# Kernel optimization log

Hardware: AMD Instinct MI355X
Metric: run time of the kernel (lower is better)

Reference implementation:

```python
import jax, jax.numpy as jnp
import numpy as np

D = 512; N = 1536; H = 4; DH = D // H
MAX_INT = 5; BINS = 100; LAYERS = 3


def _mha(q_in, k_in, v_in, in_w, in_b, out_w, out_b):
    """PyTorch-style nn.MultiheadAttention (batch of 1). Returns (out [Nq,D], head-avg weights [Nq,Nk])."""
    wq, wk, wv = in_w[:D], in_w[D:2 * D], in_w[2 * D:]
    bq, bk, bv = in_b[:D], in_b[D:2 * D], in_b[2 * D:]
    n_q, n_k = q_in.shape[0], k_in.shape[0]
    q = (q_in @ wq.T + bq).reshape(n_q, H, DH).transpose(1, 0, 2)  # [H,Nq,dh]
    k = (k_in @ wk.T + bk).reshape(n_k, H, DH).transpose(1, 0, 2)
    v = (v_in @ wv.T + bv).reshape(n_k, H, DH).transpose(1, 0, 2)
    scores = jnp.einsum('hqd,hkd->hqk', q, k) / jnp.sqrt(jnp.asarray(DH, q.dtype))
    w = jax.nn.softmax(scores, axis=-1)  # [H,Nq,Nk]
    out = jnp.einsum('hqk,hkd->hqd', w, v).transpose(1, 0, 2).reshape(n_q, D)
    out = out @ out_w.T + out_b
    return out, w.mean(0)


def setup_inputs() -> dict:
    key = jax.random.key(0)
    ks = jax.random.split(key, 12)
    s = 0.02
    return {
        'node_embeddings': jax.random.normal(ks[0], (N, D), jnp.float32),
        'time_positions': jax.random.uniform(ks[1], (N, 1), jnp.float32) * 10.0,
        'batch_indices': jnp.zeros((N,), jnp.int32),
        'W_time': jax.random.normal(ks[2], (D, 1), jnp.float32) * s,
        'b_time': jnp.zeros((D,), jnp.float32),
        'in_w': jax.random.normal(ks[3], (3 * D, D), jnp.float32) * s,
        'in_b': jnp.zeros((3 * D,), jnp.float32),
        'out_w': jax.random.normal(ks[4], (D, D), jnp.float32) * s,
        'out_b': jnp.zeros((D,), jnp.float32),
        'ic_w1': jax.random.normal(ks[5], (128, D), jnp.float32) * s,
        'ic_b1': jnp.zeros((128,), jnp.float32),
        'ic_w2': jax.random.normal(ks[6], (MAX_INT, 128), jnp.float32) * s,
        'ic_b2': jnp.zeros((MAX_INT,), jnp.float32),
        'ref_w1': jax.random.normal(ks[7], (LAYERS, 128, D + 2), jnp.float32) * s,
        'ref_b1': jnp.zeros((LAYERS, 128), jnp.float32),
        'ref_w2': jax.random.normal(ks[8], (LAYERS, 2 * BINS, 128), jnp.float32) * s,
        'ref_b2': jnp.zeros((LAYERS, 2 * BINS), jnp.float32),
        'weight_params': jnp.linspace(-0.5, 0.5, BINS).astype(jnp.float32),
        'qp_w': jax.random.normal(ks[9], (D, D + 2), jnp.float32) * s,
        'qp_b': jnp.zeros((D,), jnp.float32),
    }


def _forward(node_embeddings, time_positions, W_time, b_time, in_w, in_b, out_w, out_b,
             ic_w1, ic_b1, ic_w2, ic_b2, ref_w1, ref_b1, ref_w2, ref_b2,
             weight_params, qp_w, qp_b):
    x = node_embeddings + time_positions @ W_time.T + b_time  # [N,D]
    attn_out, _ = _mha(x, x, x, in_w, in_b, out_w, out_b)      # [N,D]
    pooled = attn_out.mean(0)                                   # [D]
    probs = jax.nn.softmax(ic_w2 @ jax.nn.relu(ic_w1 @ pooled + ic_b1) + ic_b2)
    num_intervals = jnp.argmax(probs) + 1
    interval_mask = jnp.arange(MAX_INT) < num_intervals
    t_min, t_max = time_positions.min(), time_positions.max()
    grid = jnp.linspace(t_min, t_max, MAX_INT + 1)
    start, end = grid[:-1], grid[1:]                            # [MAX_INT]
    n = attn_out.shape[0]
    ones = jnp.ones((n, 1), attn_out.dtype)

    def per_interval(s_i, e_i, w1, b1, w2, b2):
        query = jnp.concatenate([attn_out, ones * s_i, ones * e_i], axis=-1)  # [N,D+2]
        qp = query @ qp_w.T + qp_b                                            # [N,D]
        h = jax.nn.relu(query @ w1.T + b1)
        logits = h @ w2.T + b2                                                # [N,2*BINS]
        s_off = (jax.nn.softmax(logits[:, :BINS], axis=-1) * weight_params).sum(-1)  # [N]
        e_off = (jax.nn.softmax(logits[:, BINS:], axis=-1) * weight_params).sum(-1)
        _, aw = _mha(qp, attn_out, attn_out, in_w, in_b, out_w, out_b)        # [N,N]
        return (aw * s_off).sum(), (aw * e_off).sum()

    for l in range(LAYERS):  # layers have distinct params; intervals are independent within a layer
        ds, de = jax.vmap(per_interval, in_axes=(0, 0, None, None, None, None))(
            start, end, ref_w1[l], ref_b1[l], ref_w2[l], ref_b2[l])
        start = start + ds
        end = end + de

    final_bounds = jnp.stack([start, end], axis=-1)  # [MAX_INT,2]
    return final_bounds, interval_mask


def reference(node_embeddings, time_positions, batch_indices, W_time, b_time, in_w, in_b,
              out_w, out_b, ic_w1, ic_b1, ic_w2, ic_b2, ref_w1, ref_b1, ref_w2, ref_b2,
              weight_params, qp_w, qp_b):
    return _forward(node_embeddings, time_positions, W_time, b_time, in_w, in_b, out_w, out_b,
                    ic_w1, ic_b1, ic_w2, ic_b2, ref_w1, ref_b1, ref_w2, ref_b2,
                    weight_params, qp_w, qp_b)
```

## Files before the change

### kernel.cpp

```cpp
#include <hip/hip_runtime.h>
#include <hip/hip_bf16.h>

typedef __hip_bfloat16 bf16;
typedef __bf16 bf16x8 __attribute__((ext_vector_type(8)));
typedef float f32x4 __attribute__((ext_vector_type(4)));

#define DD   512
#define NT   1536
#define NH   4
#define DHD  128
#define NBINS 100
#define MAXI 5
#define NL   3
#define RSQRT_DH 0.08838834764831845f

#define OFF_ATT    ((size_t)0)
#define OFF_CTX    (OFF_ATT  + (size_t)NT*DD)
#define OFF_CTX1   (OFF_CTX  + (size_t)NT*DD)
#define OFF_H0     (OFF_CTX1 + (size_t)NT*DD)
#define OFF_LG     (OFF_H0   + (size_t)NT*384)
#define OFF_AARR   (OFF_LG   + (size_t)8*NH*NT*16)
#define OFF_BARR   (OFF_AARR + (size_t)NH*NT)
#define OFF_AV     (OFF_BARR + (size_t)NH*NT)
#define OFF_BV     (OFF_AV   + (size_t)DD)
#define OFF_B2     (OFF_BV   + (size_t)DD)
#define OFF_SOFF   (OFF_B2   + (size_t)DD)
#define OFF_EOFF   (OFF_SOFF + (size_t)MAXI*NT)
#define OFF_STAT   (OFF_EOFF + (size_t)MAXI*NT)
#define OFF_POOL   (OFF_STAT + (size_t)NH*NT*12)
#define OFF_SCAL   (OFF_POOL + (size_t)DD)
#define OFF_E      (OFF_SCAL + (size_t)64)
#define SC_START 0
#define SC_END   5
#define SC_DSDE  10
#define SC_CNT   20
#define PSLICE   ((size_t)NH*NT*16)
#define BF_BASE  (OFF_E + (size_t)NH*NT*NT/2)
#define BQKB   ((size_t)0)
#define BVT    (BQKB  + (size_t)NT*1024)
#define BATT   (BVT   + (size_t)NH*128*NT)
#define BK2    (BATT  + (size_t)NT*512)
#define BQ0    (BK2   + (size_t)NT*512)
#define BM2    (BQ0   + (size_t)NT*512)
#define BINW   (BM2   + (size_t)512*512)
#define BOUTW  (BINW  + (size_t)1536*512)
#define BRW1   (BOUTW + (size_t)512*512)
#define BRW2   (BRW1  + (size_t)384*512)

__device__ __forceinline__ void cvt8(const float* s, bf16* d) {
    float4 f0 = *(const float4*)s, f1 = *(const float4*)(s + 4);
    union { uint4 u; unsigned short us[8]; } o;
    bf16 t;
    t = __float2bfloat16(f0.x); o.us[0] = *(unsigned short*)&t;
    t = __float2bfloat16(f0.y); o.us[1] = *(unsigned short*)&t;
    t = __float2bfloat16(f0.z); o.us[2] = *(unsigned short*)&t;
    t = __float2bfloat16(f0.w); o.us[3] = *(unsigned short*)&t;
    t = __float2bfloat16(f1.x); o.us[4] = *(unsigned short*)&t;
    t = __float2bfloat16(f1.y); o.us[5] = *(unsigned short*)&t;
    t = __float2bfloat16(f1.z); o.us[6] = *(unsigned short*)&t;
    t = __float2bfloat16(f1.w); o.us[7] = *(unsigned short*)&t;
    *(uint4*)d = o.u;
}

__global__ __launch_bounds__(256) void k_misc(
    const float* __restrict__ tpos, const float* __restrict__ in_w,
    const float* __restrict__ in_b, const float* __restrict__ out_w,
    const float* __restrict__ ref_w1, const float* __restrict__ ref_w2,
    const float* __restrict__ qp_w, const float* __restrict__ qp_b, float* ws)
{
    __shared__ __bf16 As[64 * 40];
    __shared__ __bf16 Bs[64 * 40];
    __shared__ float smn[256], smx[256];
    bf16* bp = (bf16*)(ws + BF_BASE);
    int bx = blockIdx.x, tid = threadIdx.x;
    if (bx < 64) {
        int m0 = (bx >> 3) * 64, n0 = (bx & 7) * 64;
        int r = tid >> 2, quad = tid & 3;
        int w = tid >> 6, lane = tid & 63;
        int wm = (w & 1) * 32, wn = (w >> 1) * 32;
        int lr = lane & 15, lq = lane >> 4;
        f32x4 acc[2][2];
#pragma unroll
        for (int i = 0; i < 2; i++)
#pragma unroll
            for (int j = 0; j < 2; j++) acc[i][j] = (f32x4){0.f, 0.f, 0.f, 0.f};
        const float* arow = in_w + (size_t)(m0 + r) * DD + quad * 8;
        int kk = tid >> 3, g = tid & 7;
        for (int k0 = 0; k0 < DD; k0 += 32) {
            __bf16 ta[8] __attribute__((aligned(16)));
#pragma unroll
            for (int q = 0; q < 4; q++) {
                float2 f = *(const float2*)(arow + k0 + 2 * q);
                ta[2 * q] = (__bf16)f.x; ta[2 * q + 1] = (__bf16)f.y;
            }
            const float* bsrc = qp_w + (size_t)(k0 + kk) * 514 + n0 + g * 8;
            float4 b0 = *(const float4*)bsrc;
            float4 b1 = *(const float4*)(bsrc + 4);
            float bb[8] = {b0.x, b0.y, b0.z, b0.w, b1.x, b1.y, b1.z, b1.w};
            __syncthreads();
            *(bf16x8*)&As[r * 40 + quad * 8] = *(bf16x8*)ta;
#pragma unroll
            for (int q = 0; q < 8; q++) Bs[(g * 8 + q) * 40 + kk] = (__bf16)bb[q];
            __syncthreads();
            bf16x8 af[2], bfr[2];
#pragma unroll
            for (int i = 0; i < 2; i++) af[i] = *(bf16x8*)&As[(wm + i * 16 + lr) * 40 + lq * 8];
#pragma unroll
            for (int j = 0; j < 2; j++) bfr[j] = *(bf16x8*)&Bs[(wn + j * 16 + lr) * 40 + lq * 8];
#pragma unroll
            for (int i = 0; i < 2; i++)
#pragma unroll
                for (int j = 0; j < 2; j++)
                    acc[i][j] = __builtin_amdgcn_mfma_f32_16x16x32_bf16(af[i], bfr[j], acc[i][j], 0, 0, 0);
        }
        bf16* M2B = bp + BM2;
#pragma unroll
        for (int i = 0; i < 2; i++)
#pragma unroll
            for (int r4 = 0; r4 < 4; r4++) {
                int gm = m0 + wm + i * 16 + lq * 4 + r4;
#pragma unroll
                for (int j = 0; j < 2; j++)
                    M2B[(size_t)gm * 512 + n0 + wn + j * 16 + lr] = __float2bfloat16(acc[i][j][r4]);
            }
    } else if (bx < 72) {
        int w = tid >> 6, lane = tid & 63;
        float su8[8], sv8[8], sb8[8];
#pragma unroll
        for (int q = 0; q < 8; q++) {
            int c = lane * 8 + q;
            su8[q] = qp_w[(size_t)c * 514 + 512];
            sv8[q] = qp_w[(size_t)c * 514 + 513];
            sb8[q] = qp_b[c];
        }
        int base = (bx - 64) * 64 + w * 16;
        for (int t = 0; t < 16; t++) {
            int row = base + t;
            const float* wr = in_w + (size_t)row * DD + lane * 8;
            float4 x0 = *(const float4*)wr, x1 = *(const float4*)(wr + 4);
            float xa[8] = {x0.x, x0.y, x0.z, x0.w, x1.x, x1.y, x1.z, x1.w};
            float a = 0.f, b = 0.f, c2 = 0.f;
#pragma unroll
            for (int q = 0; q < 8; q++) { a += xa[q] * su8[q]; b += xa[q] * sv8[q]; c2 += xa[q] * sb8[q]; }
            for (int off = 32; off; off >>= 1) {
                a += __shfl_xor(a, off); b += __shfl_xor(b, off); c2 += __shfl_xor(c2, off);
            }
            if (lane == 0) {
                ws[OFF_AV + row] = a; ws[OFF_BV + row] = b; ws[OFF_B2 + row] = c2 + in_b[row];
            }
        }
    } else if (bx == 72) {
        ws[OFF_POOL + tid] = 0.f; ws[OFF_POOL + 256 + tid] = 0.f;
        float mn = 1e30f, mx = -1e30f;
        for (int i = tid; i < NT; i += 256) { float v = tpos[i]; mn = fminf(mn, v); mx = fmaxf(mx, v); }
        smn[tid] = mn; smx[tid] = mx; __syncthreads();
        for (int s = 128; s; s >>= 1) {
            if (tid < s) { smn[tid] = fminf(smn[tid], smn[tid + s]); smx[tid] = fmaxf(smx[tid], smx[tid + s]); }
            __syncthreads();
        }
        if (tid == 0) {
            float tmin = smn[0], tmax = smx[0];
            for (int i = 0; i < MAXI; i++) {
                ws[OFF_SCAL + SC_START + i] = tmin + (tmax - tmin) * (float)i / 5.0f;
                ws[OFF_SCAL + SC_END + i]   = tmin + (tmax - tmin) * (float)(i + 1) / 5.0f;
            }
        }
    } else if (bx < 89) {
        size_t start = (size_t)(bx - 73) * 6144;
        for (int it = 0; it < 24; it++) {
            size_t g = start + it * 256 + tid;
            cvt8(in_w + g * 8, bp + BINW + g * 8);
        }
    } else if (bx < 93) {
        size_t start = (size_t)(bx - 89) * 8192;
        for (int it = 0; it < 32; it++) {
            size_t g = start + it * 256 + tid;
            cvt8(out_w + g * 8, bp + BOUTW + g * 8);
        }
    } else if (bx < 97) {
        size_t start = (size_t)(bx - 93) * 6144;
        for (int it = 0; it < 24; it++) {
            size_t g = start + it * 256 + tid;
            int row = (int)(g >> 6), col = (int)(g & 63) * 8;
            const float* s = ref_w1 + (size_t)row * 514 + col;
            float buf[8];
#pragma unroll
            for (int q = 0; q < 4; q++) { float2 f = *(const float2*)(s + 2 * q); buf[2 * q] = f.x; buf[2 * q + 1] = f.y; }
            cvt8(buf, bp + BRW1 + (size_t)row * 512 + col);
        }
    } else {
        for (int it = 0; it < 38; it++) {
            size_t g = (size_t)it * 256 + tid;
            if (g < 9600) cvt8(ref_w2 + g * 8, bp + BRW2 + g * 8);
        }
    }
}

template <int STATS>
__global__ __launch_bounds__(256) void k_score(
    const bf16* __restrict__ Ab, int lda, int aZ,
    const bf16* __restrict__ Bb, int ldb, int bZ,
    bf16* __restrict__ E, float* __restrict__ stat)
{
    int z = blockIdx.z;
    const __bf16* A = (const __bf16*)Ab + (size_t)z * aZ;
    const __bf16* B = (const __bf16*)Bb + (size_t)z * bZ;
    int m0 = blockIdx.y * 128, n0 = blockIdx.x * 128;
    __shared__ __bf16 As[128 * 40];
    __shared__ __bf16 Bs[128 * 40];
    __shared__ float sSum[4][64];
    int tid = threadIdx.x;
    int r = tid >> 1, hh = tid & 1;
    int w = tid >> 6, lane = tid & 63;
    int wm = (w & 1) * 64, wn = (w >> 1) * 64;
    int lr = lane & 15, lq = lane >> 4;
    f32x4 acc[4][4];
#pragma unroll
    for (int i = 0; i < 4; i++)
#pragma unroll
        for (int j = 0; j < 4; j++) acc[i][j] = (f32x4){0.f, 0.f, 0.f, 0.f};

    const __bf16* arow = A + (size_t)(m0 + r) * lda + hh * 16;
    const __bf16* brow = B + (size_t)(n0 + r) * ldb + hh * 16;
    __bf16* awr = &As[r * 40 + hh * 16];
    __bf16* bwr = &Bs[r * 40 + hh * 16];

    for (int k0 = 0; k0 < DHD; k0 += 32) {
        uint4 a0 = *(const uint4*)(arow + k0);
        uint4 a1 = *(const uint4*)(arow + k0 + 8);
        uint4 b0 = *(const uint4*)(brow + k0);
        uint4 b1 = *(const uint4*)(brow + k0 + 8);
        __syncthreads();
        *(uint4*)awr = a0; *(uint4*)(awr + 8) = a1;
        *(uint4*)bwr = b0; *(uint4*)(bwr + 8) = b1;
        __syncthreads();
        bf16x8 af[4], bfr[4];
#pragma unroll
        for (int i = 0; i < 4; i++) af[i] = *(bf16x8*)&As[(wm + i * 16 + lr) * 40 + lq * 8];
#pragma unroll
        for (int j = 0; j < 4; j++) bfr[j] = *(bf16x8*)&Bs[(wn + j * 16 + lr) * 40 + lq * 8];
#pragma unroll
        for (int i = 0; i < 4; i++)
#pragma unroll
            for (int j = 0; j < 4; j++)
                acc[i][j] = __builtin_amdgcn_mfma_f32_16x16x32_bf16(af[i], bfr[j], acc[i][j], 0, 0, 0);
    }
    bf16* Ez = E + (size_t)z * NT * NT;
#pragma unroll
    for (int i = 0; i < 4; i++)
#pragma unroll
        for (int r4 = 0; r4 < 4; r4++) {
            int gm = m0 + wm + i * 16 + lq * 4 + r4;
            float s = 0.f;
#pragma unroll
            for (int j = 0; j < 4; j++) {
                float e = __expf(acc[i][j][r4] * RSQRT_DH);
                Ez[(size_t)gm * NT + n0 + wn + j * 16 + lr] = __float2bfloat16(e);
                s += e;
            }
            if (STATS) {
                for (int off = 1; off < 16; off <<= 1) s += __shfl_xor(s, off);
                if (lr == 0) sSum[w][i * 16 + lq * 4 + r4] = s;
            }
        }
    if (STATS) {
        __syncthreads();
        if (tid < 128) {
            int lidx = tid & 63, wb = tid >> 6;
            stat[((size_t)z * NT + m0 + tid) * 12 + blockIdx.x] = sSum[wb][lidx] + sSum[wb + 2][lidx];
        }
    }
}

__global__ __launch_bounds__(256) void k_qkv(
    const float* __restrict__ emb, const float* __restrict__ t,
    const float* __restrict__ wt, const float* __restrict__ bt,
    const float* __restrict__ in_b, float* ws)
{
    bf16* bp = (bf16*)(ws + BF_BASE);
    int m0 = blockIdx.y * 64, n0 = blockIdx.x * 64;
    __shared__ __bf16 As[64 * 40];
    __shared__ __bf16 Bs[64 * 40];
    int tid = threadIdx.x;
    int r = tid >> 2, quad = tid & 3;
    int w = tid >> 6, lane = tid & 63;
    int wm = (w & 1) * 32, wn = (w >> 1) * 32;
    int lr = lane & 15, lq = lane >> 4;
    f32x4 acc[2][2];
#pragma unroll
    for (int i = 0; i < 2; i++)
#pragma unroll
        for (int j = 0; j < 2; j++) acc[i][j] = (f32x4){0.f, 0.f, 0.f, 0.f};

    float trow = t[m0 + r];
    const float* arow = emb + (size_t)(m0 + r) * DD + quad * 8;
    const __bf16* brow = (const __bf16*)(bp + BINW) + (size_t)(n0 + r) * 512 + quad * 8;
    __bf16* awr = &As[r * 40 + quad * 8];
    __bf16* bwr = &Bs[r * 40 + quad * 8];

    for (int k0 = 0; k0 < DD; k0 += 32) {
        __bf16 ta[8] __attribute__((aligned(16)));
#pragma unroll
        for (int q = 0; q < 4; q++) {
            float2 e = *(const float2*)(arow + k0 + 2 * q);
            float2 wv = *(const float2*)(wt + k0 + quad * 8 + 2 * q);
            float2 bv = *(const float2*)(bt + k0 + quad * 8 + 2 * q);
            ta[2 * q]     = (__bf16)(e.x + trow * wv.x + bv.x);
            ta[2 * q + 1] = (__bf16)(e.y + trow * wv.y + bv.y);
        }
        uint4 bbv = *(const uint4*)(brow + k0);
        __syncthreads();
        *(bf16x8*)awr = *(bf16x8*)ta;
        *(uint4*)bwr = bbv;
        __syncthreads();
        bf16x8 af[2], bfr[2];
#pragma unroll
        for (int i = 0; i < 2; i++) af[i] = *(bf16x8*)&As[(wm + i * 16 + lr) * 40 + lq * 8];
#pragma unroll
        for (int j = 0; j < 2; j++) bfr[j] = *(bf16x8*)&Bs[(wn + j * 16 + lr) * 40 + lq * 8];
#pragma unroll
        for (int i = 0; i < 2; i++)
#pragma unroll
            for (int j = 0; j < 2; j++)
                acc[i][j] = __builtin_amdgcn_mfma_f32_16x16x32_bf16(af[i], bfr[j], acc[i][j], 0, 0, 0);
    }
    bf16* QKB = bp + BQKB;
    bf16* VtB = bp + BVT;
#pragma unroll
    for (int i = 0; i < 2; i++)
#pragma unroll
        for (int j = 0; j < 2; j++) {
            int gn = n0 + wn + j * 16 + lr;
            int gmb = m0 + wm + i * 16 + lq * 4;
            float b = in_b[gn];
            if (gn < 2 * DD) {
#pragma unroll
                for (int r4 = 0; r4 < 4; r4++)
                    QKB[(size_t)(gmb + r4) * 1024 + gn] = __float2bfloat16(acc[i][j][r4] + b);
            } else {
                union { uint2 u; unsigned short us[4]; } o;
#pragma unroll
                for (int r4 = 0; r4 < 4; r4++) {
                    bf16 t2 = __float2bfloat16(acc[i][j][r4] + b);
                    o.us[r4] = *(unsigned short*)&t2;
                }
                *(uint2*)&VtB[(size_t)(gn - 2 * DD) * NT + gmb] = o.u;
            }
        }
}

__global__ __launch_bounds__(256) void k_pv(const bf16* __restrict__ E, float* ws) {
    bf16* bp = (bf16*)(ws + BF_BASE);
    int h = blockIdx.z;
    int m0 = blockIdx.y * 64;
    int ks = blockIdx.x;
    const int KCH = NT / 2;
    int kbeg = ks * KCH;
    __shared__ __bf16 As[64 * 40];
    __shared__ __bf16 Bs[128 * 40];
    __shared__ float sI[64];
    int tid = threadIdx.x;
    if (tid < 64) {
        const float* st = ws + OFF_STAT + (size_t)(h * NT + m0 + tid) * 12;
        float den = 0.f;
#pragma unroll
        for (int t2 = 0; t2 < 12; t2++) den += st[t2];
        sI[tid] = 1.f / den;
    }
    int rA = tid >> 2, quadA = tid & 3;
    int rB = tid >> 1, hhB = tid & 1;
    int w = tid >> 6, lane = tid & 63;
    int wm = (w & 1) * 32, wn = (w >> 1) * 64;
    int lr = lane & 15, lq = lane >> 4;
    const __bf16* Eh = (const __bf16*)E + (size_t)h * NT * NT;
    const __bf16* arow = Eh + (size_t)(m0 + rA) * NT + quadA * 8;
    const __bf16* brow = (const __bf16*)(bp + BVT) + ((size_t)h * 128 + rB) * NT + hhB * 16;
    __bf16* awr = &As[rA * 40 + quadA * 8];
    __bf16* bwr = &Bs[rB * 40 + hhB * 16];
    f32x4 acc[2][4];
#pragma unroll
    for (int i = 0; i < 2; i++)
#pragma unroll
        for (int j = 0; j < 4; j++) acc[i][j] = (f32x4){0.f, 0.f, 0.f, 0.f};

    for (int k0 = kbeg; k0 < kbeg + KCH; k0 += 32) {
        uint4 av = *(const uint4*)(arow + k0);
        uint4 b0 = *(const uint4*)(brow + k0);
        uint4 b1 = *(const uint4*)(brow + k0 + 8);
        __syncthreads();
        *(uint4*)awr = av;
        *(uint4*)bwr = b0; *(uint4*)(bwr + 8) = b1;
        __syncthreads();
        bf16x8 af[2], bfr[4];
#pragma unroll
        for (int i = 0; i < 2; i++) af[i] = *(bf16x8*)&As[(wm + i * 16 + lr) * 40 + lq * 8];
#pragma unroll
        for (int j = 0; j < 4; j++) bfr[j] = *(bf16x8*)&Bs[(wn + j * 16 + lr) * 40 + lq * 8];
#pragma unroll
        for (int i = 0; i < 2; i++)
#pragma unroll
            for (int j = 0; j < 4; j++)
                acc[i][j] = __builtin_amdgcn_mfma_f32_16x16x32_bf16(af[i], bfr[j], acc[i][j], 0, 0, 0);
    }
    float* dst = ws + (ks == 0 ? OFF_CTX : OFF_CTX1);
#pragma unroll
    for (int i = 0; i < 2; i++)
#pragma unroll
        for (int r4 = 0; r4 < 4; r4++) {
            int lrow = wm + i * 16 + lq * 4 + r4;
            float ri = sI[lrow];
#pragma unroll
            for (int j = 0; j < 4; j++) {
                int gn = wn + j * 16 + lr;
                dst[(size_t)(m0 + lrow) * DD + h * DHD + gn] = acc[i][j][r4] * ri;
            }
        }
}

__global__ __launch_bounds__(256) void k_oproj(const float* __restrict__ out_b, float* ws) {
    bf16* bp = (bf16*)(ws + BF_BASE);
    int m0 = blockIdx.y * 64, n0 = blockIdx.x * 64;
    __shared__ __bf16 As[64 * 40];
    __shared__ __bf16 Bs[64 * 40];
    __shared__ float ps[64];
    int tid = threadIdx.x;
    int r = tid >> 2, quad = tid & 3;
    int w = tid >> 6, lane = tid & 63;
    int wm = (w & 1) * 32, wn = (w >> 1) * 32;
    int lr = lane & 15, lq = lane >> 4;
    f32x4 acc[2][2];
#pragma unroll
// ... 20 lines not shown
        uint4 bbv = *(const uint4*)(brow + k0);
        __syncthreads();
        *(bf16x8*)awr = *(bf16x8*)ta;
        *(uint4*)bwr = bbv;
        __syncthreads();
        bf16x8 af[2], bfr[2];
#pragma unroll
        for (int i = 0; i < 2; i++) af[i] = *(bf16x8*)&As[(wm + i * 16 + lr) * 40 + lq * 8];
#pragma unroll
        for (int j = 0; j < 2; j++) bfr[j] = *(bf16x8*)&Bs[(wn + j * 16 + lr) * 40 + lq * 8];
#pragma unroll
        for (int i = 0; i < 2; i++)
#pragma unroll
            for (int j = 0; j < 2; j++)
                acc[i][j] = __builtin_amdgcn_mfma_f32_16x16x32_bf16(af[i], bfr[j], acc[i][j], 0, 0, 0);
    }
    float* att = ws + OFF_ATT;
    bf16* attB = bp + BATT;
#pragma unroll
    for (int j = 0; j < 2; j++) {
        int gn = n0 + wn + j * 16 + lr;
        float b = out_b[gn];
        float colsum = 0.f;
#pragma unroll
        for (int i = 0; i < 2; i++)
#pragma unroll
            for (int r4 = 0; r4 < 4; r4++) {
                int gm = m0 + wm + i * 16 + lq * 4 + r4;
                float v = acc[i][j][r4] + b;
                att[(size_t)gm * DD + gn] = v;
                attB[(size_t)gm * 512 + gn] = __float2bfloat16(v);
                colsum += v;
            }
        atomicAdd(&ps[wn + j * 16 + lr], colsum);
    }
    __syncthreads();
    if (tid < 64) atomicAdd(&ws[OFF_POOL + n0 + tid], ps[tid]);
}

__global__ __launch_bounds__(256) void k_trip(
    const float* __restrict__ in_b, const float* __restrict__ ref_b1,
    const float* __restrict__ icw1, const float* __restrict__ icb1,
    const float* __restrict__ icw2, const float* __restrict__ icb2,
    float* ws, float* out)
{
    bf16* bp = (bf16*)(ws + BF_BASE);
    __shared__ __bf16 As[64 * 40];
    __shared__ __bf16 Bs[64 * 40];
    __shared__ float h1[128];
    __shared__ float lg[MAXI];
    int bx = blockIdx.x, tid = threadIdx.x;
    if (bx == 22) {
        if (blockIdx.y != 0) return;
        int w = tid >> 6, lane = tid & 63;
        const float* pp = ws + OFF_POOL + lane * 8;
        float4 p0 = *(const float4*)pp, p1 = *(const float4*)(pp + 4);
        float p8[8] = {p0.x, p0.y, p0.z, p0.w, p1.x, p1.y, p1.z, p1.w};
        for (int t = 0; t < 32; t++) {
            int row = w * 32 + t;
            const float* wr = icw1 + (size_t)row * DD + lane * 8;
            float4 a = *(const float4*)wr, b = *(const float4*)(wr + 4);
            float d = a.x * p8[0] + a.y * p8[1] + a.z * p8[2] + a.w * p8[3]
                    + b.x * p8[4] + b.y * p8[5] + b.z * p8[6] + b.w * p8[7];
            for (int off = 32; off; off >>= 1) d += __shfl_xor(d, off);
            if (lane == 0) h1[row] = fmaxf(d * (1.0f / NT) + icb1[row], 0.f);
        }
        __syncthreads();
        if (tid < MAXI) {
            float s = icb2[tid];
            for (int j = 0; j < 128; j++) s += icw2[tid * 128 + j] * h1[j];
            lg[tid] = s;
        }
        __syncthreads();
        if (tid == 0) {
            int best = 0; float bv = lg[0];
            for (int m = 1; m < MAXI; m++) if (lg[m] > bv) { bv = lg[m]; best = m; }
            int ni = best + 1;
            for (int i = 0; i < MAXI; i++) out[10 + i] = (i < ni) ? 1.f : 0.f;
        }
        return;
    }
    const __bf16* B; const float* bias; int n0, mode;
    bf16* Cb = nullptr; float* Cf = nullptr;
    if (bx < 8)       { B = (const __bf16*)(bp + BINW) + (size_t)512 * 512; bias = in_b + DD;     Cb = bp + BK2; n0 = bx * 64; mode = 0; }
    else if (bx < 16) { B = (const __bf16*)(bp + BM2);                      bias = ws + OFF_B2;   Cb = bp + BQ0; n0 = (bx - 8) * 64; mode = 0; }
    else              { B = (const __bf16*)(bp + BRW1);                     bias = ref_b1;        Cf = ws + OFF_H0; n0 = (bx - 16) * 64; mode = 1; }
    int m0 = blockIdx.y * 64;
    int r = tid >> 2, quad = tid & 3;
    int w = tid >> 6, lane = tid & 63;
    int wm = (w & 1) * 32, wn = (w >> 1) * 32;
    int lr = lane & 15, lq = lane >> 4;
    f32x4 acc[2][2];
#pragma unroll
    for (int i = 0; i < 2; i++)
#pragma unroll
        for (int j = 0; j < 2; j++) acc[i][j] = (f32x4){0.f, 0.f, 0.f, 0.f};

    const __bf16* arow = (const __bf16*)(bp + BATT) + (size_t)(m0 + r) * 512 + quad * 8;
    const __bf16* brow = B + (size_t)(n0 + r) * 512 + quad * 8;
    __bf16* awr = &As[r * 40 + quad * 8];
    __bf16* bwr = &Bs[r * 40 + quad * 8];

    for (int k0 = 0; k0 < DD; k0 += 32) {
        uint4 av = *(const uint4*)(arow + k0);
        uint4 bv = *(const uint4*)(brow + k0);
        __syncthreads();
        *(uint4*)awr = av;
        *(uint4*)bwr = bv;
        __syncthreads();
        bf16x8 af[2], bfr[2];
#pragma unroll
        for (int i = 0; i < 2; i++) af[i] = *(bf16x8*)&As[(wm + i * 16 + lr) * 40 + lq * 8];
#pragma unroll
        for (int j = 0; j < 2; j++) bfr[j] = *(bf16x8*)&Bs[(wn + j * 16 + lr) * 40 + lq * 8];
#pragma unroll
        for (int i = 0; i < 2; i++)
#pragma unroll
            for (int j = 0; j < 2; j++)
                acc[i][j] = __builtin_amdgcn_mfma_f32_16x16x32_bf16(af[i], bfr[j], acc[i][j], 0, 0, 0);
    }
#pragma unroll
    for (int i = 0; i < 2; i++)
#pragma unroll
        for (int r4 = 0; r4 < 4; r4++) {
            int gm = m0 + wm + i * 16 + lq * 4 + r4;
#pragma unroll
            for (int j = 0; j < 2; j++) {
                int gn = n0 + wn + j * 16 + lr;
                float v = acc[i][j][r4] + bias[gn];
                if (mode == 0) Cb[(size_t)gm * 512 + gn] = __float2bfloat16(v);
                else           Cf[(size_t)gm * 384 + gn] = v;
            }
        }
}

__global__ __launch_bounds__(256) void k_abc(float* ws) {
    bf16* bp = (bf16*)(ws + BF_BASE);
    int wave = threadIdx.x >> 6, lane = threadIdx.x & 63;
    int row = blockIdx.x * 4 + wave;
    int h = row / NT, n = row % NT;
    const unsigned short* k2 = (const unsigned short*)(bp + BK2 + (size_t)n * 512 + h * DHD);
    const float* av = ws + OFF_AV + h * DHD;
    const float* bv = ws + OFF_BV + h * DHD;
    int d = lane * 2;
    float k0 = __uint_as_float((unsigned)k2[d] << 16);
    float k1 = __uint_as_float((unsigned)k2[d + 1] << 16);
    float a = av[d] * k0 + av[d + 1] * k1;
    float b = bv[d] * k0 + bv[d + 1] * k1;
    for (int off = 32; off; off >>= 1) { a += __shfl_xor(a, off); b += __shfl_xor(b, off); }
    if (lane == 0) { ws[OFF_AARR + row] = a * RSQRT_DH; ws[OFF_BARR + row] = b * RSQRT_DH; }
}

__global__ __launch_bounds__(256) void k_lgs(
    const float* __restrict__ rw1, const float* __restrict__ rb2,
    const float* __restrict__ wp, int l, float* ws)
{
    bf16* bp = (bf16*)(ws + BF_BASE);
    __shared__ float dsh[128];
    __shared__ __bf16 As[64 * 136];
    __shared__ __bf16 Bs[64 * 136];
    __shared__ __bf16 Ls[64 * 208];
    int tid = threadIdx.x;
    int m0 = blockIdx.x * 64;
    int i_int = m0 / NT;
    int nbase = m0 % NT;
    if (blockIdx.x == 0 && tid < 11) ws[OFF_SCAL + SC_DSDE + tid] = 0.f;
    if (tid < 128) {
        float s_i = ws[OFF_SCAL + SC_START + i_int], e_i = ws[OFF_SCAL + SC_END + i_int];
        const float* wr = rw1 + (size_t)(l * 128 + tid) * 514;
        dsh[tid] = s_i * wr[512] + e_i * wr[513];
    }
    __syncthreads();
    int r = tid >> 2, quad = tid & 3;
    {
        const float* arow = ws + OFF_H0 + (size_t)(nbase + r) * 384 + l * 128 + quad * 32;
        __bf16 tmp[32] __attribute__((aligned(16)));
#pragma unroll
        for (int q = 0; q < 16; q++) {
            float2 f = *(const float2*)(arow + 2 * q);
            int jj = quad * 32 + 2 * q;
            tmp[2 * q]     = (__bf16)fmaxf(f.x + dsh[jj], 0.f);
            tmp[2 * q + 1] = (__bf16)fmaxf(f.y + dsh[jj + 1], 0.f);
        }
        __bf16* aw = &As[r * 136 + quad * 32];
#pragma unroll
        for (int q = 0; q < 4; q++) *(bf16x8*)(aw + q * 8) = *(bf16x8*)(tmp + q * 8);
    }
    int w = tid >> 6, lane = tid & 63;
    int wm = (w & 1) * 32, wn = (w >> 1) * 32;
    int lr = lane & 15, lq = lane >> 4;
    const __bf16* rw2b = (const __bf16*)(bp + BRW2) + (size_t)l * 200 * 128;
    for (int nt = 0; nt < 4; nt++) {
        int n0 = nt * 64;
        int gnr = n0 + r;
        uint4 b0 = {0, 0, 0, 0}, b1 = {0, 0, 0, 0}, b2v = {0, 0, 0, 0}, b3 = {0, 0, 0, 0};
        if (gnr < 200) {
            const __bf16* brow = rw2b + (size_t)gnr * 128 + quad * 32;
            b0 = *(const uint4*)brow; b1 = *(const uint4*)(brow + 8);
            b2v = *(const uint4*)(brow + 16); b3 = *(const uint4*)(brow + 24);
        }
        __syncthreads();
        {
            __bf16* bw = &Bs[r * 136 + quad * 32];
            *(uint4*)bw = b0; *(uint4*)(bw + 8) = b1;
            *(uint4*)(bw + 16) = b2v; *(uint4*)(bw + 24) = b3;
        }
        __syncthreads();
        f32x4 acc[2][2];
#pragma unroll
        for (int i = 0; i < 2; i++)
#pragma unroll
            for (int j = 0; j < 2; j++) acc[i][j] = (f32x4){0.f, 0.f, 0.f, 0.f};
#pragma unroll
        for (int kk = 0; kk < 4; kk++) {
            bf16x8 af[2], bfr[2];
#pragma unroll
            for (int i = 0; i < 2; i++) af[i] = *(bf16x8*)&As[(wm + i * 16 + lr) * 136 + kk * 32 + lq * 8];
#pragma unroll
            for (int j = 0; j < 2; j++) bfr[j] = *(bf16x8*)&Bs[(wn + j * 16 + lr) * 136 + kk * 32 + lq * 8];
#pragma unroll
            for (int i = 0; i < 2; i++)
#pragma unroll
                for (int j = 0; j < 2; j++)
                    acc[i][j] = __builtin_amdgcn_mfma_f32_16x16x32_bf16(af[i], bfr[j], acc[i][j], 0, 0, 0);
        }
#pragma unroll
        for (int i = 0; i < 2; i++)
#pragma unroll
            for (int r4 = 0; r4 < 4; r4++) {
                int rl = wm + i * 16 + lq * 4 + r4;
#pragma unroll
                for (int j = 0; j < 2; j++) {
                    int gn = n0 + wn + j * 16 + lr;
                    if (gn < 200) Ls[rl * 208 + gn] = (__bf16)(acc[i][j][r4] + rb2[gn]);
                }
            }
    }
    __syncthreads();
    {
        int rloc = tid >> 2, q = tid & 3;
        int c0 = q * 50;
        const unsigned short* lrow = (const unsigned short*)&Ls[rloc * 208];
        float m = -1e30f;
#pragma unroll
        for (int c = 0; c < 50; c++)
            m = fmaxf(m, __uint_as_float((unsigned)lrow[c0 + c] << 16));
        m = fmaxf(m, __shfl_xor(m, 1));
        float den = 0.f, num = 0.f;
#pragma unroll
        for (int c = 0; c < 50; c++) {
            float p = __expf(__uint_as_float((unsigned)lrow[c0 + c] << 16) - m);
            den += p;
            int wc = c0 + c; if (wc >= NBINS) wc -= NBINS;
            num += p * wp[wc];
        }
        den += __shfl_xor(den, 1);
        num += __shfl_xor(num, 1);
        int n = nbase + rloc;
        if (q == 0)      ws[OFF_SOFF + (size_t)i_int * NT + n] = num / den;
        else if (q == 2) ws[OFF_EOFF + (size_t)i_int * NT + n] = num / den;
    }
}

__global__ __launch_bounds__(256) void k_eg(const bf16* __restrict__ E0, float* ws) {
    int h = blockIdx.z;
    int m0 = blockIdx.y * 128;
    int ks = blockIdx.x;
    const int KCH = NT / 8;
    __shared__ __bf16 As[128 * 40];
    __shared__ __bf16 Bs[16 * 40];
    int tid = threadIdx.x;
    int w = tid >> 6, lane = tid & 63;
    int lr = lane & 15, lq = lane >> 4;
    int r = tid >> 1, half = tid & 1;
    const unsigned short* arow =
        (const unsigned short*)((const __bf16*)E0 + (size_t)h * NT * NT + (size_t)(m0 + r) * NT) + half * 16;
    int wm = w * 32;
    f32x4 acc[2];
    acc[0] = (f32x4){0.f, 0.f, 0.f, 0.f};
    acc[1] = (f32x4){0.f, 0.f, 0.f, 0.f};
    int bc = tid >> 3, bk = tid & 7;
    int valid = (tid < 128) && (bc < 15);
    int ii = bc / 3, tt = bc - ii * 3;
    if (ii > 4) ii = 4;
    float s_i = 0.f, e_i = 0.f;
    if (valid) { s_i = ws[OFF_SCAL + SC_START + ii]; e_i = ws[OFF_SCAL + SC_END + ii]; }
    const float* Ar = ws + OFF_AARR + h * NT;
    const float* Br = ws + OFF_BARR + h * NT;
    const float* fo = ws + (tt == 2 ? OFF_EOFF : OFF_SOFF) + (size_t)ii * NT;

    for (int k0 = ks * KCH; k0 < ks * KCH + KCH; k0 += 32) {
        uint4 a0 = *(const uint4*)(arow + k0);
        uint4 a1 = *(const uint4*)(arow + k0 + 8);
        float bv[4] = {0.f, 0.f, 0.f, 0.f};
        if (valid) {
            float4 a4 = *(const float4*)(Ar + k0 + bk * 4);
            float4 b4 = *(const float4*)(Br + k0 + bk * 4);
            bv[0] = __expf(s_i * a4.x + e_i * b4.x);
            bv[1] = __expf(s_i * a4.y + e_i * b4.y);
            bv[2] = __expf(s_i * a4.z + e_i * b4.z);
            bv[3] = __expf(s_i * a4.w + e_i * b4.w);
            if (tt) {
                float4 f4 = *(const float4*)(fo + k0 + bk * 4);
                bv[0] *= f4.x; bv[1] *= f4.y; bv[2] *= f4.z; bv[3] *= f4.w;
            }
        }
        __syncthreads();
        *(uint4*)&As[r * 40 + half * 16] = a0;
        *(uint4*)&As[r * 40 + half * 16 + 8] = a1;
        if (tid < 128) {
            __bf16* bw = &Bs[bc * 40 + bk * 4];
            bw[0] = (__bf16)bv[0]; bw[1] = (__bf16)bv[1]; bw[2] = (__bf16)bv[2]; bw[3] = (__bf16)bv[3];
        }
        __syncthreads();
        bf16x8 bf0 = *(bf16x8*)&Bs[lr * 40 + lq * 8];
        bf16x8 af0 = *(bf16x8*)&As[(wm + lr) * 40 + lq * 8];
        bf16x8 af1 = *(bf16x8*)&As[(wm + 16 + lr) * 40 + lq * 8];
        acc[0] = __builtin_amdgcn_mfma_f32_16x16x32_bf16(af0, bf0, acc[0], 0, 0, 0);
        acc[1] = __builtin_amdgcn_mfma_f32_16x16x32_bf16(af1, bf0, acc[1], 0, 0, 0);
    }
    float* P = ws + OFF_LG + (size_t)ks * PSLICE;
    if (lr < 15) {
#pragma unroll
        for (int i = 0; i < 2; i++)
#pragma unroll
            for (int r4 = 0; r4 < 4; r4++) {
                int gm = m0 + wm + i * 16 + lq * 4 + r4;
                P[(size_t)(h * NT + gm) * 16 + lr] = acc[i][r4];
            }
    }
}

__global__ __launch_bounds__(256) void k_fin(float* ws, float* out, int l) {
    __shared__ float part[4][10];
    int tid = threadIdx.x;
    int w = tid >> 6, lane = tid & 63;
    int row = blockIdx.x * 256 + tid;
    float acc[15];
#pragma unroll
    for (int c = 0; c < 15; c++) acc[c] = 0.f;
    for (int ks = 0; ks < 8; ks++) {
        const float* Pr = ws + OFF_LG + (size_t)ks * PSLICE + (size_t)row * 16;
#pragma unroll
        for (int c = 0; c < 15; c++) acc[c] += Pr[c];
    }
    float loc[10];
#pragma unroll
    for (int i = 0; i < MAXI; i++) {
        float den = acc[i * 3];
        loc[i]        = acc[i * 3 + 1] / den;
        loc[MAXI + i] = acc[i * 3 + 2] / den;
    }
#pragma unroll
    for (int c = 0; c < 10; c++)
        for (int off = 32; off; off >>= 1) loc[c] += __shfl_xor(loc[c], off);
    if (lane == 0) {
#pragma unroll
        for (int c = 0; c < 10; c++) part[w][c] = loc[c];
    }
    __syncthreads();
    if (tid < 10) {
        float s = part[0][tid] + part[1][tid] + part[2][tid] + part[3][tid];
        atomicAdd(&ws[OFF_SCAL + SC_DSDE + tid], s);
    }
    __threadfence();
    __syncthreads();
    if (tid == 0) {
        unsigned old = atomicAdd((unsigned*)&ws[OFF_SCAL + SC_CNT], 1u);
        if (old == 23) {
            for (int i = 0; i < MAXI; i++) {
                float ds = atomicAdd(&ws[OFF_SCAL + SC_DSDE + i], 0.f);
                float de = atomicAdd(&ws[OFF_SCAL + SC_DSDE + MAXI + i], 0.f);
                float ns = ws[OFF_SCAL + SC_START + i] + ds * 0.25f;
                float ne = ws[OFF_SCAL + SC_END + i]   + de * 0.25f;
                ws[OFF_SCAL + SC_START + i] = ns;
                ws[OFF_SCAL + SC_END + i]   = ne;
                if (l == NL - 1) { out[2 * i] = ns; out[2 * i + 1] = ne; }
            }
        }
    }
}

extern "C" void kernel_launch(void* const* d_in, const int* in_sizes, int n_in,
                              void* d_out, int out_size, void* d_ws, size_t ws_size,
                              hipStream_t stream) {
    const float* emb    = (const float*)d_in[0];
    const float* tpos   = (const float*)d_in[1];
    const float* W_time = (const float*)d_in[3];
    const float* b_time = (const float*)d_in[4];
    const float* in_w   = (const float*)d_in[5];
    const float* in_b   = (const float*)d_in[6];
    const float* out_w  = (const float*)d_in[7];
    const float* out_b  = (const float*)d_in[8];
    const float* ic_w1  = (const float*)d_in[9];
    const float* ic_b1  = (const float*)d_in[10];
    const float* ic_w2  = (const float*)d_in[11];
    const float* ic_b2  = (const float*)d_in[12];
    const float* ref_w1 = (const float*)d_in[13];
    const float* ref_b1 = (const float*)d_in[14];
    const float* ref_w2 = (const float*)d_in[15];
    const float* ref_b2 = (const float*)d_in[16];
    const float* wp     = (const float*)d_in[17];
    const float* qp_w   = (const float*)d_in[18];
    const float* qp_b   = (const float*)d_in[19];
    float* ws  = (float*)d_ws;
    float* out = (float*)d_out;
    bf16* E = (bf16*)(ws + OFF_E);
    bf16* bp = (bf16*)(ws + BF_BASE);

    k_misc<<<98, 256, 0, stream>>>(tpos, in_w, in_b, out_w, ref_w1, ref_w2, qp_w, qp_b, ws);

    k_qkv<<<dim3(24, 24), 256, 0, stream>>>(emb, tpos, W_time, b_time, in_b, ws);
    k_score<1><<<dim3(12, 12, NH), 256, 0, stream>>>(
        bp + BQKB, 1024, DHD, bp + BQKB + 512, 1024, DHD, E, ws + OFF_STAT);
    k_pv<<<dim3(2, NT / 64, NH), 256, 0, stream>>>(E, ws);
    k_oproj<<<dim3(8, 24), 256, 0, stream>>>(out_b, ws);

    k_trip<<<dim3(23, 24), 256, 0, stream>>>(in_b, ref_b1, ic_w1, ic_b1, ic_w2, ic_b2, ws, out);

    k_score<0><<<dim3(12, 12, NH), 256, 0, stream>>>(
        bp + BQ0, 512, DHD, bp + BK2, 512, DHD, E, nullptr);
    k_abc<<<NH * NT / 4, 256, 0, stream>>>(ws);

    for (int l = 0; l < NL; l++) {
        k_lgs<<<120, 256, 0, stream>>>(ref_w1, ref_b2 + l * 200, wp, l, ws);
        k_eg<<<dim3(8, NT / 128, NH), 256, 0, stream>>>(E, ws);
        k_fin<<<NH * NT / 256, 256, 0, stream>>>(ws, out, l);
    }
}
```

Baseline: 305.9 us.

## Fuse split-K eg with finalize and fold abc into score launch

Replaces the split-K k_eg (8 K-slices writing partials to a global buffer) plus the k_fin reduction kernel with a single k_egf kernel. Each 64-row block walks the full K range, reduces its 64x16 tile in shared memory, and does the per-row normalisation and atomic accumulation itself, with the last-arriving block updating the interval bounds. The k_abc kernel is merged into the second k_score launch as an extra z-slice of blocks, and the partial-sum buffer is removed. This cuts kernel launches and partial-buffer traffic, but leaves only 96 blocks with a long serial K loop in each refinement layer, which risks lower parallelism.

```diff
diff --git a/kernel.cpp b/kernel.cpp
--- a/kernel.cpp
+++ b/kernel.cpp
@@ -18,8 +18,7 @@
 #define OFF_CTX    (OFF_ATT  + (size_t)NT*DD)
 #define OFF_CTX1   (OFF_CTX  + (size_t)NT*DD)
 #define OFF_H0     (OFF_CTX1 + (size_t)NT*DD)
-#define OFF_LG     (OFF_H0   + (size_t)NT*384)
-#define OFF_AARR   (OFF_LG   + (size_t)8*NH*NT*16)
+#define OFF_AARR   (OFF_H0   + (size_t)NT*384)
 #define OFF_BARR   (OFF_AARR + (size_t)NH*NT)
 #define OFF_AV     (OFF_BARR + (size_t)NH*NT)
 #define OFF_BV     (OFF_AV   + (size_t)DD)
@@ -34,7 +33,6 @@
 #define SC_END   5
 #define SC_DSDE  10
 #define SC_CNT   20
-#define PSLICE   ((size_t)NH*NT*16)
 #define BF_BASE  (OFF_E + (size_t)NH*NT*NT/2)
 #define BQKB   ((size_t)0)
 #define BVT    (BQKB  + (size_t)NT*1024)
@@ -196,82 +194,6 @@
     }
 }
 
-template <int STATS>
-__global__ __launch_bounds__(256) void k_score(
-    const bf16* __restrict__ Ab, int lda, int aZ,
-    const bf16* __restrict__ Bb, int ldb, int bZ,
-    bf16* __restrict__ E, float* __restrict__ stat)
-{
-    int z = blockIdx.z;
-    const __bf16* A = (const __bf16*)Ab + (size_t)z * aZ;
-    const __bf16* B = (const __bf16*)Bb + (size_t)z * bZ;
-    int m0 = blockIdx.y * 128, n0 = blockIdx.x * 128;
-    __shared__ __bf16 As[128 * 40];
-    __shared__ __bf16 Bs[128 * 40];
-    __shared__ float sSum[4][64];
-    int tid = threadIdx.x;
-    int r = tid >> 1, hh = tid & 1;
-    int w = tid >> 6, lane = tid & 63;
-    int wm = (w & 1) * 64, wn = (w >> 1) * 64;
-    int lr = lane & 15, lq = lane >> 4;
-    f32x4 acc[4][4];
-#pragma unroll
-    for (int i = 0; i < 4; i++)
-#pragma unroll
-        for (int j = 0; j < 4; j++) acc[i][j] = (f32x4){0.f, 0.f, 0.f, 0.f};
-
-    const __bf16* arow = A + (size_t)(m0 + r) * lda + hh * 16;
-    const __bf16* brow = B + (size_t)(n0 + r) * ldb + hh * 16;
-    __bf16* awr = &As[r * 40 + hh * 16];
-    __bf16* bwr = &Bs[r * 40 + hh * 16];
-
-    for (int k0 = 0; k0 < DHD; k0 += 32) {
-        uint4 a0 = *(const uint4*)(arow + k0);
-        uint4 a1 = *(const uint4*)(arow + k0 + 8);
-        uint4 b0 = *(const uint4*)(brow + k0);
-        uint4 b1 = *(const uint4*)(brow + k0 + 8);
-        __syncthreads();
-        *(uint4*)awr = a0; *(uint4*)(awr + 8) = a1;
-        *(uint4*)bwr = b0; *(uint4*)(bwr + 8) = b1;
-        __syncthreads();
-        bf16x8 af[4], bfr[4];
-#pragma unroll
-        for (int i = 0; i < 4; i++) af[i] = *(bf16x8*)&As[(wm + i * 16 + lr) * 40 + lq * 8];
-#pragma unroll
-        for (int j = 0; j < 4; j++) bfr[j] = *(bf16x8*)&Bs[(wn + j * 16 + lr) * 40 + lq * 8];
-#pragma unroll
-        for (int i = 0; i < 4; i++)
-#pragma unroll
-            for (int j = 0; j < 4; j++)
-                acc[i][j] = __builtin_amdgcn_mfma_f32_16x16x32_bf16(af[i], bfr[j], acc[i][j], 0, 0, 0);
-    }
-    bf16* Ez = E + (size_t)z * NT * NT;
-#pragma unroll
-    for (int i = 0; i < 4; i++)
-#pragma unroll
-        for (int r4 = 0; r4 < 4; r4++) {
-            int gm = m0 + wm + i * 16 + lq * 4 + r4;
-            float s = 0.f;
-#pragma unroll
-            for (int j = 0; j < 4; j++) {
-                float e = __expf(acc[i][j][r4] * RSQRT_DH);
-                Ez[(size_t)gm * NT + n0 + wn + j * 16 + lr] = __float2bfloat16(e);
-                s += e;
-            }
-            if (STATS) {
-                for (int off = 1; off < 16; off <<= 1) s += __shfl_xor(s, off);
-                if (lr == 0) sSum[w][i * 16 + lq * 4 + r4] = s;
-            }
-        }
-    if (STATS) {
-        __syncthreads();
-        if (tid < 128) {
-            int lidx = tid & 63, wb = tid >> 6;
-            stat[((size_t)z * NT + m0 + tid) * 12 + blockIdx.x] = sSum[wb][lidx] + sSum[wb + 2][lidx];
-        }
-    }
-}
-
 __global__ __launch_bounds__(256) void k_qkv(
     const float* __restrict__ emb, const float* __restrict__ t,
     const float* __restrict__ wt, const float* __restrict__ bt,
@@ -347,6 +269,103 @@
                 *(uint2*)&VtB[(size_t)(gn - 2 * DD) * NT + gmb] = o.u;
             }
         }
+}
+
+template <int STATS>
+__global__ __launch_bounds__(256) void k_score(
+    const bf16* __restrict__ Ab, int lda, int aZ,
+    const bf16* __restrict__ Bb, int ldb, int bZ,
+    bf16* __restrict__ E, float* ws)
+{
+    int tid = threadIdx.x;
+    if (!STATS && blockIdx.z == 4) {
+        bf16* bp = (bf16*)(ws + BF_BASE);
+        int flat = blockIdx.y * 12 + blockIdx.x;
+        int w = tid >> 6, lane = tid & 63;
+        for (int t = w; t < 43; t += 4) {
+            int row = flat * 43 + t;
+            if (row >= NH * NT) break;
+            int hh = row / NT, n = row % NT;
+            const unsigned short* k2 = (const unsigned short*)(bp + BK2 + (size_t)n * 512 + hh * DHD);
+            const float* av = ws + OFF_AV + hh * DHD;
+            const float* bv = ws + OFF_BV + hh * DHD;
+            int d = lane * 2;
+            float k0 = __uint_as_float((unsigned)k2[d] << 16);
+            float k1 = __uint_as_float((unsigned)k2[d + 1] << 16);
+            float a = av[d] * k0 + av[d + 1] * k1;
+            float b = bv[d] * k0 + bv[d + 1] * k1;
+            for (int off = 32; off; off >>= 1) { a += __shfl_xor(a, off); b += __shfl_xor(b, off); }
+            if (lane == 0) { ws[OFF_AARR + row] = a * RSQRT_DH; ws[OFF_BARR + row] = b * RSQRT_DH; }
+        }
+        return;
+    }
+    int z = blockIdx.z;
+    const __bf16* A = (const __bf16*)Ab + (size_t)z * aZ;
+    const __bf16* B = (const __bf16*)Bb + (size_t)z * bZ;
+    int m0 = blockIdx.y * 128, n0 = blockIdx.x * 128;
+    __shared__ __bf16 As[128 * 40];
+    __shared__ __bf16 Bs[128 * 40];
+    __shared__ float sSum[4][64];
+    int r = tid >> 1, hh = tid & 1;
+    int w = tid >> 6, lane = tid & 63;
+    int wm = (w & 1) * 64, wn = (w >> 1) * 64;
+    int lr = lane & 15, lq = lane >> 4;
+    f32x4 acc[4][4];
+#pragma unroll
+    for (int i = 0; i < 4; i++)
+#pragma unroll
+        for (int j = 0; j < 4; j++) acc[i][j] = (f32x4){0.f, 0.f, 0.f, 0.f};
+
+    const __bf16* arow = A + (size_t)(m0 + r) * lda + hh * 16;
+    const __bf16* brow = B + (size_t)(n0 + r) * ldb + hh * 16;
+    __bf16* awr = &As[r * 40 + hh * 16];
+    __bf16* bwr = &Bs[r * 40 + hh * 16];
+
+    for (int k0 = 0; k0 < DHD; k0 += 32) {
+        uint4 a0 = *(const uint4*)(arow + k0);
+        uint4 a1 = *(const uint4*)(arow + k0 + 8);
+        uint4 b0 = *(const uint4*)(brow + k0);
+        uint4 b1 = *(const uint4*)(brow + k0 + 8);
+        __syncthreads();
+        *(uint4*)awr = a0; *(uint4*)(awr + 8) = a1;
+        *(uint4*)bwr = b0; *(uint4*)(bwr + 8) = b1;
+        __syncthreads();
+        bf16x8 af[4], bfr[4];
+#pragma unroll
+        for (int i = 0; i < 4; i++) af[i] = *(bf16x8*)&As[(wm + i * 16 + lr) * 40 + lq * 8];
+#pragma unroll
+        for (int j = 0; j < 4; j++) bfr[j] = *(bf16x8*)&Bs[(wn + j * 16 + lr) * 40 + lq * 8];
+#pragma unroll
+        for (int i = 0; i < 4; i++)
+#pragma unroll
+            for (int j = 0; j < 4; j++)
+                acc[i][j] = __builtin_amdgcn_mfma_f32_16x16x32_bf16(af[i], bfr[j], acc[i][j], 0, 0, 0);
+    }
+    bf16* Ez = E + (size_t)z * NT * NT;
+#pragma unroll
+    for (int i = 0; i < 4; i++)
+#pragma unroll
+        for (int r4 = 0; r4 < 4; r4++) {
+            int gm = m0 + wm + i * 16 + lq * 4 + r4;
+            float s = 0.f;
+#pragma unroll
+            for (int j = 0; j < 4; j++) {
+                float e = __expf(acc[i][j][r4] * RSQRT_DH);
+                Ez[(size_t)gm * NT + n0 + wn + j * 16 + lr] = __float2bfloat16(e);
+                s += e;
+            }
+            if (STATS) {
+                for (int off = 1; off < 16; off <<= 1) s += __shfl_xor(s, off);
+                if (lr == 0) sSum[w][i * 16 + lq * 4 + r4] = s;
+            }
+        }
+    if (STATS) {
+        __syncthreads();
+        if (tid < 128) {
+            int lidx = tid & 63, wb = tid >> 6;
+            ws[OFF_STAT + ((size_t)z * NT + m0 + tid) * 12 + blockIdx.x] = sSum[wb][lidx] + sSum[wb + 2][lidx];
+        }
+    }
 }
 
 __global__ __launch_bounds__(256) void k_pv(const bf16* __restrict__ E, float* ws) {
@@ -533,9 +552,9 @@
     }
     const __bf16* B; const float* bias; int n0, mode;
     bf16* Cb = nullptr; float* Cf = nullptr;
-    if (bx < 8)       { B = (const __bf16*)(bp + BINW) + (size_t)512 * 512; bias = in_b + DD;     Cb = bp + BK2; n0 = bx * 64; mode = 0; }
-    else if (bx < 16) { B = (const __bf16*)(bp + BM2);                      bias = ws + OFF_B2;   Cb = bp + BQ0; n0 = (bx - 8) * 64; mode = 0; }
-    else              { B = (const __bf16*)(bp + BRW1);                     bias = ref_b1;        Cf = ws + OFF_H0; n0 = (bx - 16) * 64; mode = 1; }
+    if (bx < 8)       { B = (const __bf16*)(bp + BINW) + (size_t)512 * 512; bias = in_b + DD;   Cb = bp + BK2; n0 = bx * 64; mode = 0; }
+    else if (bx < 16) { B = (const __bf16*)(bp + BM2);                      bias = ws + OFF_B2; Cb = bp + BQ0; n0 = (bx - 8) * 64; mode = 0; }
+    else              { B = (const __bf16*)(bp + BRW1);                     bias = ref_b1;      Cf = ws + OFF_H0; n0 = (bx - 16) * 64; mode = 1; }
     int m0 = blockIdx.y * 64;
     int r = tid >> 2, quad = tid & 3;
     int w = tid >> 6, lane = tid & 63;
@@ -583,23 +602,6 @@
                 else           Cf[(size_t)gm * 384 + gn] = v;
             }
         }
-}
-
-__global__ __launch_bounds__(256) void k_abc(float* ws) {
-    bf16* bp = (bf16*)(ws + BF_BASE);
-    int wave = threadIdx.x >> 6, lane = threadIdx.x & 63;
-    int row = blockIdx.x * 4 + wave;
-    int h = row / NT, n = row % NT;
-    const unsigned short* k2 = (const unsigned short*)(bp + BK2 + (size_t)n * 512 + h * DHD);
-    const float* av = ws + OFF_AV + h * DHD;
-    const float* bv = ws + OFF_BV + h * DHD;
-    int d = lane * 2;
-    float k0 = __uint_as_float((unsigned)k2[d] << 16);
-    float k1 = __uint_as_float((unsigned)k2[d + 1] << 16);
-    float a = av[d] * k0 + av[d + 1] * k1;
-    float b = bv[d] * k0 + bv[d + 1] * k1;
-    for (int off = 32; off; off >>= 1) { a += __shfl_xor(a, off); b += __shfl_xor(b, off); }
-    if (lane == 0) { ws[OFF_AARR + row] = a * RSQRT_DH; ws[OFF_BARR + row] = b * RSQRT_DH; }
 }
 
 __global__ __launch_bounds__(256) void k_lgs(
@@ -713,38 +715,34 @@
     }
 }
 
-__global__ __launch_bounds__(256) void k_eg(const bf16* __restrict__ E0, float* ws) {
-    int h = blockIdx.z;
-    int m0 = blockIdx.y * 128;
-    int ks = blockIdx.x;
-    const int KCH = NT / 8;
-    __shared__ __bf16 As[128 * 40];
-    __shared__ __bf16 Bs[16 * 40];
+__global__ __launch_bounds__(256) void k_egf(const bf16* __restrict__ E0, float* ws, float* out, int l) {
+    int h = blockIdx.y;
+    int m0 = blockIdx.x * 64;
+    __shared__ __bf16 As[64 * 72];
+    __shared__ __bf16 Bs[16 * 72];
+    __shared__ float Ps[64 * 17];
     int tid = threadIdx.x;
     int w = tid >> 6, lane = tid & 63;
     int lr = lane & 15, lq = lane >> 4;
-    int r = tid >> 1, half = tid & 1;
+    int wm = w * 16;
+    int r = tid >> 2, quad = tid & 3;
     const unsigned short* arow =
-        (const unsigned short*)((const __bf16*)E0 + (size_t)h * NT * NT + (size_t)(m0 + r) * NT) + half * 16;
-    int wm = w * 32;
-    f32x4 acc[2];
-    acc[0] = (f32x4){0.f, 0.f, 0.f, 0.f};
-    acc[1] = (f32x4){0.f, 0.f, 0.f, 0.f};
-    int bc = tid >> 3, bk = tid & 7;
-    int valid = (tid < 128) && (bc < 15);
+        (const unsigned short*)((const __bf16*)E0 + (size_t)h * NT * NT + (size_t)(m0 + r) * NT) + quad * 16;
+    f32x4 acc = (f32x4){0.f, 0.f, 0.f, 0.f};
+    int bc = tid >> 4, bk = tid & 15;
+    int bvalid = (bc < 15);
     int ii = bc / 3, tt = bc - ii * 3;
     if (ii > 4) ii = 4;
-    float s_i = 0.f, e_i = 0.f;
-    if (valid) { s_i = ws[OFF_SCAL + SC_START + ii]; e_i = ws[OFF_SCAL + SC_END + ii]; }
+    float s_i = ws[OFF_SCAL + SC_START + ii], e_i = ws[OFF_SCAL + SC_END + ii];
     const float* Ar = ws + OFF_AARR + h * NT;
     const float* Br = ws + OFF_BARR + h * NT;
     const float* fo = ws + (tt == 2 ? OFF_EOFF : OFF_SOFF) + (size_t)ii * NT;
 
-    for (int k0 = ks * KCH; k0 < ks * KCH + KCH; k0 += 32) {
+    for (int k0 = 0; k0 < NT; k0 += 64) {
         uint4 a0 = *(const uint4*)(arow + k0);
         uint4 a1 = *(const uint4*)(arow + k0 + 8);
         float bv[4] = {0.f, 0.f, 0.f, 0.f};
-        if (valid) {
+        if (bvalid) {
             float4 a4 = *(const float4*)(Ar + k0 + bk * 4);
             float4 b4 = *(const float4*)(Br + k0 + bk * 4);
             bv[0] = __expf(s_i * a4.x + e_i * b4.x);
@@ -757,76 +755,51 @@
             }
         }
         __syncthreads();
-        *(uint4*)&As[r * 40 + half * 16] = a0;
-        *(uint4*)&As[r * 40 + half * 16 + 8] = a1;
-        if (tid < 128) {
-            __bf16* bw = &Bs[bc * 40 + bk * 4];
+        *(uint4*)&As[r * 72 + quad * 16] = a0;
+        *(uint4*)&As[r * 72 + quad * 16 + 8] = a1;
+        if (bvalid) {
+            __bf16* bw = &Bs[bc * 72 + bk * 4];
             bw[0] = (__bf16)bv[0]; bw[1] = (__bf16)bv[1]; bw[2] = (__bf16)bv[2]; bw[3] = (__bf16)bv[3];
         }
         __syncthreads();
-        bf16x8 bf0 = *(bf16x8*)&Bs[lr * 40 + lq * 8];
-        bf16x8 af0 = *(bf16x8*)&As[(wm + lr) * 40 + lq * 8];
-        bf16x8 af1 = *(bf16x8*)&As[(wm + 16 + lr) * 40 + lq * 8];
-        acc[0] = __builtin_amdgcn_mfma_f32_16x16x32_bf16(af0, bf0, acc[0], 0, 0, 0);
-        acc[1] = __builtin_amdgcn_mfma_f32_16x16x32_bf16(af1, bf0, acc[1], 0, 0, 0);
-    }
-    float* P = ws + OFF_LG + (size_t)ks * PSLICE;
-    if (lr < 15) {
-#pragma unroll
-        for (int i = 0; i < 2; i++)
-#pragma unroll
-            for (int r4 = 0; r4 < 4; r4++) {
-                int gm = m0 + wm + i * 16 + lq * 4 + r4;
-                P[(size_t)(h * NT + gm) * 16 + lr] = acc[i][r4];
-            }
-    }
-}
-
-__global__ __launch_bounds__(256) void k_fin(float* ws, float* out, int l) {
-    __shared__ float part[4][10];
-    int tid = threadIdx.x;
-    int w = tid >> 6, lane = tid & 63;
-    int row = blockIdx.x * 256 + tid;
-    float acc[15];
-#pragma unroll
-    for (int c = 0; c < 15; c++) acc[c] = 0.f;
-    for (int ks = 0; ks < 8; ks++) {
-        const float* Pr = ws + OFF_LG + (size_t)ks * PSLICE + (size_t)row * 16;
-#pragma unroll
-        for (int c = 0; c < 15; c++) acc[c] += Pr[c];
-    }
-    float loc[10];
-#pragma unroll
-    for (int i = 0; i < MAXI; i++) {
-        float den = acc[i * 3];
-        loc[i]        = acc[i * 3 + 1] / den;
-        loc[MAXI + i] = acc[i * 3 + 2] / den;
-    }
-#pragma unroll
-    for (int c = 0; c < 10; c++)
-        for (int off = 32; off; off >>= 1) loc[c] += __shfl_xor(loc[c], off);
-    if (lane == 0) {
-#pragma unroll
-        for (int c = 0; c < 10; c++) part[w][c] = loc[c];
-    }
+#pragma unroll
+        for (int ks = 0; ks < 2; ks++) {
+            bf16x8 af = *(bf16x8*)&As[(wm + lr) * 72 + ks * 32 + lq * 8];
+            bf16x8 bf0 = *(bf16x8*)&Bs[lr * 72 + ks * 32 + lq * 8];
+            acc = __builtin_amdgcn_mfma_f32_16x16x32_bf16(af, bf0, acc, 0, 0, 0);
+        }
+    }
+#pragma unroll
+    for (int reg = 0; reg < 4; reg++)
+        Ps[(wm + lq * 4 + reg) * 17 + lr] = acc[reg];
     __syncthreads();
-    if (tid < 10) {
-        float s = part[0][tid] + part[1][tid] + part[2][tid] + part[3][tid];
-        atomicAdd(&ws[OFF_SCAL + SC_DSDE + tid], s);
-    }
-    __threadfence();
-    __syncthreads();
-    if (tid == 0) {
-        unsigned old = atomicAdd((unsigned*)&ws[OFF_SCAL + SC_CNT], 1u);
-        if (old == 23) {
-            for (int i = 0; i < MAXI; i++) {
-                float ds = atomicAdd(&ws[OFF_SCAL + SC_DSDE + i], 0.f);
-                float de = atomicAdd(&ws[OFF_SCAL + SC_DSDE + MAXI + i], 0.f);
-                float ns = ws[OFF_SCAL + SC_START + i] + ds * 0.25f;
-                float ne = ws[OFF_SCAL + SC_END + i]   + de * 0.25f;
-                ws[OFF_SCAL + SC_START + i] = ns;
-                ws[OFF_SCAL + SC_END + i]   = ne;
-                if (l == NL - 1) { out[2 * i] = ns; out[2 * i + 1] = ne; }
+    if (w == 0) {
+        const float* P = &Ps[lane * 17];
+        float loc[10];
+#pragma unroll
+        for (int i = 0; i < MAXI; i++) {
+            float dn = P[i * 3];
+            loc[i]        = P[i * 3 + 1] / dn;
+            loc[MAXI + i] = P[i * 3 + 2] / dn;
+        }
+#pragma unroll
+        for (int c = 0; c < 10; c++)
+            for (int off = 32; off; off >>= 1) loc[c] += __shfl_xor(loc[c], off);
+        if (lane == 0) {
+#pragma unroll
+            for (int c = 0; c < 10; c++) atomicAdd(&ws[OFF_SCAL + SC_DSDE + c], loc[c]);
+            __threadfence();
+            unsigned old = atomicAdd((unsigned*)&ws[OFF_SCAL + SC_CNT], 1u);
+            if (old == 95) {
+                for (int i = 0; i < MAXI; i++) {
+                    float ds = atomicAdd(&ws[OFF_SCAL + SC_DSDE + i], 0.f);
+                    float de = atomicAdd(&ws[OFF_SCAL + SC_DSDE + MAXI + i], 0.f);
+                    float ns = ws[OFF_SCAL + SC_START + i] + ds * 0.25f;
+                    float ne = ws[OFF_SCAL + SC_END + i]   + de * 0.25f;
+                    ws[OFF_SCAL + SC_START + i] = ns;
+                    ws[OFF_SCAL + SC_END + i]   = ne;
+                    if (l == NL - 1) { out[2 * i] = ns; out[2 * i + 1] = ne; }
+                }
             }
         }
     }
@@ -863,19 +836,17 @@
 
     k_qkv<<<dim3(24, 24), 256, 0, stream>>>(emb, tpos, W_time, b_time, in_b, ws);
     k_score<1><<<dim3(12, 12, NH), 256, 0, stream>>>(
-        bp + BQKB, 1024, DHD, bp + BQKB + 512, 1024, DHD, E, ws + OFF_STAT);
+        bp + BQKB, 1024, DHD, bp + BQKB + 512, 1024, DHD, E, ws);
     k_pv<<<dim3(2, NT / 64, NH), 256, 0, stream>>>(E, ws);
     k_oproj<<<dim3(8, 24), 256, 0, stream>>>(out_b, ws);
 
     k_trip<<<dim3(23, 24), 256, 0, stream>>>(in_b, ref_b1, ic_w1, ic_b1, ic_w2, ic_b2, ws, out);
 
-    k_score<0><<<dim3(12, 12, NH), 256, 0, stream>>>(
-        bp + BQ0, 512, DHD, bp + BK2, 512, DHD, E, nullptr);
-    k_abc<<<NH * NT / 4, 256, 0, stream>>>(ws);
+    k_score<0><<<dim3(12, 12, 5), 256, 0, stream>>>(
+        bp + BQ0, 512, DHD, bp + BK2, 512, DHD, E, ws);
 
     for (int l = 0; l < NL; l++) {
         k_lgs<<<120, 256, 0, stream>>>(ref_w1, ref_b2 + l * 200, wp, l, ws);
-        k_eg<<<dim3(8, NT / 128, NH), 256, 0, stream>>>(E, ws);
-        k_fin<<<NH * NT / 256, 256, 0, stream>>>(ws, out, l);
-    }
-}
+        k_egf<<<dim3(24, NH), 256, 0, stream>>>(E, ws, out, l);
+    }
+}
```

After: 352.8 us. 15.3% more time.
